# Optimization experiments

Measured on AMD Instinct MI355X. Metric: run time of the kernel, lower is better.

The kernel has to match this reference:

```python
import jax, jax.numpy as jnp
import numpy as np

BATCH, GROUPS, ARITY, OUT_DIM = 1024, 512, 4, 64


def _high_order_act(X, params):
    # X: [B, G, K]; params: [G, 2**K, D]
    A_ind = jnp.argsort(X, axis=2)                                   # [B,G,K] int
    A_sort = jnp.take_along_axis(X, A_ind, axis=2)                   # sorted values
    # barycentric-style coefficients: smallest value, then successive gaps
    coef = jnp.concatenate(
        [A_sort[:, :, :1], A_sort[:, :, 1:] - A_sort[:, :, :-1]], axis=2
    )                                                                 # [B,G,K]
    # reversed cumulative sum of 2**A_ind -> vertex index into 2**K table
    pow2 = jnp.left_shift(jnp.int32(1), A_ind.astype(jnp.int32))      # [B,G,K]
    idx = jnp.flip(jnp.cumsum(jnp.flip(pow2, axis=2), axis=2), axis=2)  # [B,G,K]
    G = params.shape[0]
    g_idx = jnp.arange(G)[None, :, None]                              # [1,G,1]
    pg = params[g_idx, idx]                                           # [B,G,K,D] gather
    return jnp.einsum('bgk,bgkd->bgd', coef, pg)                      # [B,G,D]


def setup_inputs() -> dict:
    key = jax.random.key(0)
    k1, k2 = jax.random.split(key)
    X = jax.random.normal(k1, (BATCH, GROUPS, ARITY), dtype=jnp.float32)
    params = jax.random.normal(k2, (GROUPS, 2 ** ARITY, OUT_DIM), dtype=jnp.float32)
    return {"X": X, "params": params}


def reference(X, params):
    return _high_order_act(X, params)
```

## Files before the change

kernel.cpp:

```cpp
#include <hip/hip_runtime.h>

#define BATCH   1024
#define GROUPS  512
#define ARITY   4
#define OUT_DIM 64

__global__ __launch_bounds__(256) void hoact_kernel(
    const float4* __restrict__ X4,
    const float4* __restrict__ P4,
    float4*       __restrict__ O4)
{
    const int tid = blockIdx.x * blockDim.x + threadIdx.x;
    const int t   = tid & 15;
    const int bg  = tid >> 4;
    const int g   = bg & (GROUPS - 1);

    const float4 x = X4[bg];
    float v0 = x.x, v1 = x.y, v2 = x.z, v3 = x.w;
    int   i0 = 0,   i1 = 1,   i2 = 2,   i3 = 3;

#define CSWAP(a, b, ia, ib)                         \
    {                                               \
        const bool sw = (a) > (b);                  \
        const float ta = (a), tb = (b);             \
        const int  tia = (ia), tib = (ib);          \
        (a)  = sw ? tb  : ta;  (b)  = sw ? ta  : tb;  \
        (ia) = sw ? tib : tia; (ib) = sw ? tia : tib; \
    }
    CSWAP(v0, v1, i0, i1);
    CSWAP(v2, v3, i2, i3);
    CSWAP(v0, v2, i0, i2);
    CSWAP(v1, v3, i1, i3);
    CSWAP(v1, v2, i1, i2);
#undef CSWAP

    const float c0 = v0;
    const float c1 = v1 - v0;
    const float c2 = v2 - v1;
    const float c3 = v3 - v2;

    const int e3 = 1 << i3;
    const int e2 = e3 + (1 << i2);
    const int e1 = e2 + (1 << i1);

    const float4* base = P4 + (size_t)g * (16 * 16) + t;
    const float4 p0 = base[15 * 16];
    const float4 p1 = base[e1 * 16];
    const float4 p2 = base[e2 * 16];
    const float4 p3 = base[e3 * 16];

    float4 o;
    o.x = c0 * p0.x + c1 * p1.x + c2 * p2.x + c3 * p3.x;
    o.y = c0 * p0.y + c1 * p1.y + c2 * p2.y + c3 * p3.y;
    o.z = c0 * p0.z + c1 * p1.z + c2 * p2.z + c3 * p3.z;
    o.w = c0 * p0.w + c1 * p1.w + c2 * p2.w + c3 * p3.w;

    O4[tid] = o;
}

extern "C" void kernel_launch(void* const* d_in, const int* in_sizes, int n_in,
                              void* d_out, int out_size, void* d_ws, size_t ws_size,
                              hipStream_t stream) {
    const float4* X4 = (const float4*)d_in[0];
    const float4* P4 = (const float4*)d_in[1];
    float4*       O4 = (float4*)d_out;

    const int total_threads = BATCH * GROUPS * (OUT_DIM / 4);
    const int block = 256;
    const int grid  = total_threads / block;

    hipLaunchKernelGGL(hoact_kernel, dim3(grid), dim3(block), 0, stream,
                       X4, P4, O4);
}
```

Baseline: 168.7 us.

## Pack sort indices into float mantissa bits and compute two float4 outputs per thread

Each thread now produces two float4 outputs, which halves the thread count and the redundant per-thread X load and sort work. The sorting network now tags each value's low two mantissa bits with its original index, so it can sort with fminf/fmaxf and recover the indices afterwards. This drops the separate index swaps. The tagging slightly perturbs the values used as coefficients and can change tie ordering, a small accuracy risk.

```diff
diff --git a/kernel.cpp b/kernel.cpp
--- a/kernel.cpp
+++ b/kernel.cpp
@@ -11,28 +11,33 @@
     float4*       __restrict__ O4)
 {
     const int tid = blockIdx.x * blockDim.x + threadIdx.x;
-    const int t   = tid & 15;
-    const int bg  = tid >> 4;
+    const int t   = tid & 7;
+    const int bg  = tid >> 3;
     const int g   = bg & (GROUPS - 1);
 
     const float4 x = X4[bg];
-    float v0 = x.x, v1 = x.y, v2 = x.z, v3 = x.w;
-    int   i0 = 0,   i1 = 1,   i2 = 2,   i3 = 3;
 
-#define CSWAP(a, b, ia, ib)                         \
-    {                                               \
-        const bool sw = (a) > (b);                  \
-        const float ta = (a), tb = (b);             \
-        const int  tia = (ia), tib = (ib);          \
-        (a)  = sw ? tb  : ta;  (b)  = sw ? ta  : tb;  \
-        (ia) = sw ? tib : tia; (ib) = sw ? tia : tib; \
+    float v0 = __uint_as_float((__float_as_uint(x.x) & ~3u) | 0u);
+    float v1 = __uint_as_float((__float_as_uint(x.y) & ~3u) | 1u);
+    float v2 = __uint_as_float((__float_as_uint(x.z) & ~3u) | 2u);
+    float v3 = __uint_as_float((__float_as_uint(x.w) & ~3u) | 3u);
+
+#define CSWAP(a, b)                                  \
+    {                                                \
+        const float lo = fminf((a), (b));            \
+        const float hi = fmaxf((a), (b));            \
+        (a) = lo; (b) = hi;                          \
     }
-    CSWAP(v0, v1, i0, i1);
-    CSWAP(v2, v3, i2, i3);
-    CSWAP(v0, v2, i0, i2);
-    CSWAP(v1, v3, i1, i3);
-    CSWAP(v1, v2, i1, i2);
+    CSWAP(v0, v1);
+    CSWAP(v2, v3);
+    CSWAP(v0, v2);
+    CSWAP(v1, v3);
+    CSWAP(v1, v2);
 #undef CSWAP
+
+    const int i1 = __float_as_uint(v1) & 3;
+    const int i2 = __float_as_uint(v2) & 3;
+    const int i3 = __float_as_uint(v3) & 3;
 
     const float c0 = v0;
     const float c1 = v1 - v0;
@@ -43,19 +48,28 @@
     const int e2 = e3 + (1 << i2);
     const int e1 = e2 + (1 << i1);
 
-    const float4* base = P4 + (size_t)g * (16 * 16) + t;
-    const float4 p0 = base[15 * 16];
-    const float4 p1 = base[e1 * 16];
-    const float4 p2 = base[e2 * 16];
-    const float4 p3 = base[e3 * 16];
+    const float4* base = P4 + (size_t)g * 256 + t;
+    const float4 p0a = base[15 * 16];
+    const float4 p0b = base[15 * 16 + 8];
+    const float4 p1a = base[e1 * 16];
+    const float4 p1b = base[e1 * 16 + 8];
+    const float4 p2a = base[e2 * 16];
+    const float4 p2b = base[e2 * 16 + 8];
+    const float4 p3a = base[e3 * 16];
+    const float4 p3b = base[e3 * 16 + 8];
 
-    float4 o;
-    o.x = c0 * p0.x + c1 * p1.x + c2 * p2.x + c3 * p3.x;
-    o.y = c0 * p0.y + c1 * p1.y + c2 * p2.y + c3 * p3.y;
-    o.z = c0 * p0.z + c1 * p1.z + c2 * p2.z + c3 * p3.z;
-    o.w = c0 * p0.w + c1 * p1.w + c2 * p2.w + c3 * p3.w;
+    float4 oa, ob;
+    oa.x = c0 * p0a.x + c1 * p1a.x + c2 * p2a.x + c3 * p3a.x;
+    oa.y = c0 * p0a.y + c1 * p1a.y + c2 * p2a.y + c3 * p3a.y;
+    oa.z = c0 * p0a.z + c1 * p1a.z + c2 * p2a.z + c3 * p3a.z;
+    oa.w = c0 * p0a.w + c1 * p1a.w + c2 * p2a.w + c3 * p3a.w;
+    ob.x = c0 * p0b.x + c1 * p1b.x + c2 * p2b.x + c3 * p3b.x;
+    ob.y = c0 * p0b.y + c1 * p1b.y + c2 * p2b.y + c3 * p3b.y;
+    ob.z = c0 * p0b.z + c1 * p1b.z + c2 * p2b.z + c3 * p3b.z;
+    ob.w = c0 * p0b.w + c1 * p1b.w + c2 * p2b.w + c3 * p3b.w;
 
-    O4[tid] = o;
+    O4[bg * 16 + t]     = oa;
+    O4[bg * 16 + t + 8] = ob;
 }
 
 extern "C" void kernel_launch(void* const* d_in, const int* in_sizes, int n_in,
@@ -65,7 +79,7 @@
     const float4* P4 = (const float4*)d_in[1];
     float4*       O4 = (float4*)d_out;
 
-    const int total_threads = BATCH * GROUPS * (OUT_DIM / 4);
+    const int total_threads = BATCH * GROUPS * (OUT_DIM / 8);
     const int block = 256;
     const int grid  = total_threads / block;
 
```

Result: faster. 163.3 us (-3.2%).
